# Kernel tuning notes

Measured on AMD Instinct MI355X. Metric: run time of the kernel, lower is better.

The kernel has to match this reference:

```python
import jax, jax.numpy as jnp
import numpy as np

N, E, DIN, DH, R = 50000, 1600000, 128, 128, 3


def setup_inputs() -> dict:
    key = jax.random.key(0)
    ks = jax.random.split(key, 32)
    inp = {}
    inp["x"] = jax.random.normal(ks[0], (N, DIN), jnp.float32)
    inp["h_prev"] = jax.random.normal(ks[1], (N, DH), jnp.float32)
    inp["edge_index"] = jax.random.randint(ks[2], (2, E), 0, N)
    inp["node_role"] = jax.random.randint(ks[3], (N,), 0, R)
    i = 4
    for name, din, has_b in (("xz", DIN, True), ("hz", DH, False), ("xr", DIN, True), ("hr", DH, False), ("xh", DIN, True), ("hh", DH, False)):
        inp[name + "_W"] = jax.random.normal(ks[i], (din, DH), jnp.float32) / np.float32(np.sqrt(din)); i += 1
        inp[name + "_Wg"] = jax.random.normal(ks[i], (R, DH), jnp.float32) * np.float32(0.1); i += 1
        inp[name + "_bg"] = jnp.zeros((R, DH), jnp.float32)
        inp[name + "_S"] = jax.random.normal(ks[i], (R, DH, DH), jnp.float32) / np.float32(np.sqrt(DH)); i += 1
        if has_b:
            inp[name + "_b"] = jnp.zeros((R, DH), jnp.float32)
    return inp


def _role_conv(x, W, Wg, bg, S, b, row, col, node_role):
    # x: [N, din] -> transformed features [N, DH]
    xt = x @ W
    r = node_role[row]                                  # role of source node per edge
    g = jax.nn.sigmoid(Wg[r] + bg[r])                   # [Etot, DH] role gate
    msg = xt[row] * g
    if b is not None:
        msg = msg + b[r]
    n = x.shape[0]
    summed = jax.ops.segment_sum(msg, col, num_segments=n)
    cnt = jax.ops.segment_sum(jnp.ones((row.shape[0],), xt.dtype), col, num_segments=n)
    aggr = summed / jnp.maximum(cnt, 1.0)[:, None]      # scatter_mean (self-loops ensure cnt>=1)
    # per-role self transform: out[i] = xt[i] @ S[role[i]] + aggr[i]
    out = aggr
    for nr in range(R):
        out = out + jnp.where((node_role == nr)[:, None], xt @ S[nr], jnp.float32(0.0))
    return jax.nn.relu(out)


def reference(x, edge_index, h_prev, node_role,
              xz_W, xz_Wg, xz_bg, xz_S, xz_b,
              hz_W, hz_Wg, hz_bg, hz_S,
              xr_W, xr_Wg, xr_bg, xr_S, xr_b,
              hr_W, hr_Wg, hr_bg, hr_S,
              xh_W, xh_Wg, xh_bg, xh_S, xh_b,
              hh_W, hh_Wg, hh_bg, hh_S):
    n = x.shape[0]
    loops = jnp.arange(n, dtype=edge_index.dtype)
    row = jnp.concatenate([edge_index[0], loops])       # add_self_loops appended at end
    col = jnp.concatenate([edge_index[1], loops])

    z = jax.nn.sigmoid(_role_conv(x, xz_W, xz_Wg, xz_bg, xz_S, xz_b, row, col, node_role)
                       + _role_conv(h_prev, hz_W, hz_Wg, hz_bg, hz_S, None, row, col, node_role))
    r = jax.nn.sigmoid(_role_conv(x, xr_W, xr_Wg, xr_bg, xr_S, xr_b, row, col, node_role)
                       + _role_conv(h_prev, hr_W, hr_Wg, hr_bg, hr_S, None, row, col, node_role))
    h_tilde = jnp.tanh(_role_conv(x, xh_W, xh_Wg, xh_bg, xh_S, xh_b, row, col, node_role)
                       + _role_conv(r * h_prev, hh_W, hh_Wg, hh_bg, hh_S, None, row, col, node_role))
    h_new = z * h_prev + (1.0 - z) * h_tilde
    return h_new
```

## Files before the change

### kernel.cpp

```cpp
#include <hip/hip_runtime.h>


typedef __bf16 bf16;
typedef __bf16 bf16x8 __attribute__((ext_vector_type(8)));
typedef float  f32x4  __attribute__((ext_vector_type(4)));
typedef float  f32x2  __attribute__((ext_vector_type(2)));
typedef unsigned char u8;

#define DH 128

__device__ __forceinline__ float sigmoidf_(float x) { return 1.0f / (1.0f + expf(-x)); }

__global__ __launch_bounds__(256) void hist_kernel(const int* __restrict__ ei, const int* __restrict__ role,
                                                   int* __restrict__ cnt3, int* __restrict__ rolecnt,
                                                   int E, int N)
{
  int i = blockIdx.x * 256 + threadIdx.x;
  int lane = threadIdx.x & 63;
  int r = (i < N) ? role[i] : -1;
  #pragma unroll
  for (int rr = 0; rr < 3; ++rr) {
    unsigned long long mask = __ballot(r == rr);
    if (lane == 0 && mask) atomicAdd(&rolecnt[rr], __popcll(mask));
  }
  if (i < E + N) {
    int src, dst;
    if (i < E) { src = ei[i]; dst = ei[E + i]; } else { src = i - E; dst = i - E; }
    int rs = (i < E) ? role[src] : r;
    if (i >= E) rs = role[i - E];
    atomicAdd(&cnt3[dst * 3 + rs], 1);
  }
}

__global__ __launch_bounds__(1024) void scan1_kernel(const int* __restrict__ cnt, int* __restrict__ off,
                                                     int* __restrict__ bsum, int n)
{
  __shared__ int wsum[16];
  int t = threadIdx.x, lane = t & 63, w = t >> 6;
  int idx = blockIdx.x * 1024 + t;
  int v = (idx < n) ? cnt[idx] : 0;
  int s = v;
  #pragma unroll
  for (int d = 1; d < 64; d <<= 1) { int u = __shfl_up(s, d); if (lane >= d) s += u; }
  if (lane == 63) wsum[w] = s;
  __syncthreads();
  if (w == 0 && lane < 16) {
    int ws = wsum[lane];
    #pragma unroll
    for (int d = 1; d < 16; d <<= 1) { int u = __shfl_up(ws, d); if (lane >= d) ws += u; }
    wsum[lane] = ws;
  }
  __syncthreads();
  int inc = ((w > 0) ? wsum[w - 1] : 0) + s;
  if (idx < n) off[idx + 1] = inc;
  if (t == 1023) bsum[blockIdx.x] = inc;
}

__global__ void scan2_kernel(int* __restrict__ bsum, int nb, const int* __restrict__ rolecnt,
                             int* __restrict__ rolefill, int* __restrict__ roleinfo)
{
  int lane = threadIdx.x;
  int carry = 0;
  for (int base = 0; base < nb; base += 64) {
    int v = (base + lane < nb) ? bsum[base + lane] : 0;
    int s = v;
    #pragma unroll
    for (int d = 1; d < 64; d <<= 1) { int u = __shfl_up(s, d); if (lane >= d) s += u; }
    if (base + lane < nb) bsum[base + lane] = carry + s - v;
    carry += __shfl(s, 63);
  }
  if (lane == 0) {
    int c0 = rolecnt[0], c1 = rolecnt[1], c2 = rolecnt[2];
    int s1 = (c0 + 255) & ~255;
    int s2 = s1 + ((c1 + 255) & ~255);
    int mp = s2 + ((c2 + 255) & ~255);
    rolefill[0] = 0; rolefill[1] = s1; rolefill[2] = s2;
    roleinfo[0] = s1; roleinfo[1] = s2;
    roleinfo[2] = c0;      roleinfo[3] = s1 - c0;
    roleinfo[4] = s1 + c1; roleinfo[5] = s2 - s1 - c1;
    roleinfo[6] = s2 + c2; roleinfo[7] = mp - s2 - c2;
  }
}

__global__ __launch_bounds__(1024) void scan3_kernel(int* __restrict__ off, int* __restrict__ fill,
                                                     const int* __restrict__ bsum, int n)
{
  int idx = blockIdx.x * 1024 + threadIdx.x;
  if (idx == 0) { off[0] = 0; fill[0] = 0; }
  if (idx < n) {
    int v = off[idx + 1] + bsum[blockIdx.x];
    off[idx + 1] = v;
    if (idx + 1 < n) fill[idx + 1] = v;
  }
}

__global__ void bucketinit_kernel(const int* __restrict__ off3, int* __restrict__ bucketfill,
                                  int NB, int W, int N)
{
  int b = blockIdx.x * 256 + threadIdx.x;
  if (b < NB) {
    int d = min(b * W, N);
    bucketfill[b] = off3[d * 3];
  }
}

__global__ __launch_bounds__(256) void partition_kernel(
    const int* __restrict__ ei, const int* __restrict__ spos,
    const int* __restrict__ roleinfo, int* __restrict__ bucketfill,
    int2* __restrict__ recs, int E, int N, int shiftB)
{
  __shared__ int lcnt[256], lbase[256];
  const int base = blockIdx.x * 4096;
  const int s1 = roleinfo[0], s2 = roleinfo[1];
  lcnt[threadIdx.x] = 0;
  __syncthreads();
  int myb[16], mybin[16], myt[16];
  #pragma unroll
  for (int k = 0; k < 16; ++k) {
    int i = base + k * 256 + threadIdx.x;
    myb[k] = -1;
    if (i < E + N) {
      int src, dst;
      if (i < E) { src = ei[i]; dst = ei[E + i]; } else { src = i - E; dst = i - E; }
      int t = spos[src];
      int r = (t >= s2) ? 2 : (t >= s1) ? 1 : 0;
      myb[k] = dst >> shiftB;
      mybin[k] = dst * 3 + r;
      myt[k] = t;
      atomicAdd(&lcnt[myb[k]], 1);
    }
  }
  __syncthreads();
  int c = lcnt[threadIdx.x];
  lbase[threadIdx.x] = (c > 0) ? atomicAdd(&bucketfill[threadIdx.x], c) : 0;
  __syncthreads();
  lcnt[threadIdx.x] = 0;
  __syncthreads();
  #pragma unroll
  for (int k = 0; k < 16; ++k) {
    if (myb[k] >= 0) {
      int slot = atomicAdd(&lcnt[myb[k]], 1);
      recs[lbase[myb[k]] + slot] = make_int2(mybin[k], myt[k]);
    }
  }
}

__global__ __launch_bounds__(1024) void binscatter_kernel(
    const int2* __restrict__ recs, const int* __restrict__ off3,
    int* __restrict__ fill3, int* __restrict__ ssrc, int W, int N)
{
  int b = blockIdx.x;
  int d0 = min(b * W, N), d1 = min((b + 1) * W, N);
  int s = off3[d0 * 3], e = off3[d1 * 3];
  for (int i = s + threadIdx.x; i < e; i += 1024) {
    int2 rec = recs[i];
    int pz = atomicAdd(&fill3[rec.x], 1);
    ssrc[pz] = rec.y;
  }
}

__global__ __launch_bounds__(256) void permscatter_kernel(const int* __restrict__ role, int* __restrict__ rolefill,
                                                          int* __restrict__ spos, int* __restrict__ sposinv, int N)
{
  int i = blockIdx.x * 256 + threadIdx.x;
  int lane = threadIdx.x & 63;
  int r = (i < N) ? role[i] : -1;
  #pragma unroll
  for (int rr = 0; rr < 3; ++rr) {
    unsigned long long mask = __ballot(r == rr);
    if (!mask) continue;
    int base = 0;
    if (lane == 0) base = atomicAdd(&rolefill[rr], __popcll(mask));
    base = __shfl(base, 0);
    if (r == rr) {
      int rank = (int)__popcll(mask & ((1ull << lane) - 1ull));
      int pos = base + rank;
      spos[i] = pos;
      sposinv[pos] = i;
    }
  }
}

__global__ __launch_bounds__(256) void zeropad_kernel(const int* __restrict__ roleinfo,
                                                      bf16* __restrict__ Ax, bf16* __restrict__ Ah)
{
  int id = blockIdx.x * 256 + threadIdx.x;
  int a = id / 49152, rem = id % 49152;
  int gp = rem / 16384, r2 = rem % 16384;
  int rr = r2 >> 6, c = r2 & 63;
  int gs = roleinfo[2 + gp * 2], gl = roleinfo[3 + gp * 2];
  if (rr < gl) {
    int row = gs + rr;
    size_t unit = (size_t)(row >> 4) * 1024 + c * 16 + (row & 15);
    bf16x8 z = {};
    ((bf16x8*)(a == 0 ? Ax : Ah))[unit] = z;
  }
}

__global__ __launch_bounds__(256) void prep_xh_kernel(const float* __restrict__ x, const float* __restrict__ h,
                                                      const int* __restrict__ spos, u8* __restrict__ xq8,
                                                      bf16* __restrict__ Ax, bf16* __restrict__ Ah, int N)
{
  int g = blockIdx.x * 256 + threadIdx.x;
  if (g >= N * 32) return;
  int n = g >> 5, j = g & 31;
  int t = spos[n];
  const float* src = (j < 16) ? (x + (size_t)n * 128 + (j << 3))
                              : (h + (size_t)n * 128 + ((j - 16) << 3));
  float4 v0 = ((const float4*)src)[0];
  float4 v1 = ((const float4*)src)[1];
  int lo = __builtin_amdgcn_cvt_pk_fp8_f32(v0.x, v0.y, 0, false);
  lo = __builtin_amdgcn_cvt_pk_fp8_f32(v0.z, v0.w, lo, true);
  int hi = __builtin_amdgcn_cvt_pk_fp8_f32(v1.x, v1.y, 0, false);
  hi = __builtin_amdgcn_cvt_pk_fp8_f32(v1.z, v1.w, hi, true);
  *(int2*)(xq8 + (size_t)t * 256 + j * 8) = make_int2(lo, hi);
  bf16x8 o;
  o[0] = (bf16)v0.x; o[1] = (bf16)v0.y; o[2] = (bf16)v0.z; o[3] = (bf16)v0.w;
  o[4] = (bf16)v1.x; o[5] = (bf16)v1.y; o[6] = (bf16)v1.z; o[7] = (bf16)v1.w;
  size_t unit = (size_t)(t >> 4) * 1024 + (48 + (j & 15)) * 16 + (t & 15);
  ((bf16x8*)(j < 16 ? Ax : Ah))[unit] = o;
}

struct PrepW { const float* W[6]; const float* Wg[6]; const float* bg[6]; };
__global__ __launch_bounds__(256) void prep_wf_kernel(PrepW pw, bf16* __restrict__ Wf)
{
  int idx = blockIdx.x * 256 + threadIdx.x;
  if (idx >= 294912) return;
  int cv = idx / 49152, pos = idx % 49152;
  int ks4q = pos >> 10;
  int col = (pos >> 3) & 127, j = pos & 7;
  int k = (ks4q >> 2) * 32 + (ks4q & 3) * 8 + j;
  int r = k >> 7, kk = k & 127;
  float g = sigmoidf_(pw.Wg[cv][r * 128 + col] + pw.bg[cv][r * 128 + col]);
  Wf[idx] = (bf16)(pw.W[cv][kk * 128 + col] * g);
}

struct PrepP { const float* W[6]; const float* S[6]; };
__global__ __launch_bounds__(128) void prep_pf_kernel(PrepP pp, bf16* __restrict__ Pf)
{
  int b = blockIdx.x;
  int cv = b / 384, rem = b % 384;
  int r = rem >> 7, kp = rem & 127;
  int col = threadIdx.x;
  const float* W = pp.W[cv] + (size_t)kp * 128;
  const float* S = pp.S[cv] + (size_t)r * 16384;
  float sum = 0.f;
  #pragma unroll 4
  for (int j2 = 0; j2 < 128; ++j2) sum += W[j2] * S[j2 * 128 + col];
  size_t o = (size_t)(cv * 3 + r) * 16384 + ((size_t)(kp >> 3) * 128 + col) * 8 + (kp & 7);
  Pf[o] = (bf16)sum;
}

#define ACCUM16(U, d) do { f32x2 f_;                                                   \
  f_ = __builtin_amdgcn_cvt_pk_f32_fp8((d).x, false); U[0]  += f_[0]; U[1]  += f_[1];  \
  f_ = __builtin_amdgcn_cvt_pk_f32_fp8((d).x, true);  U[2]  += f_[0]; U[3]  += f_[1];  \
  f_ = __builtin_amdgcn_cvt_pk_f32_fp8((d).y, false); U[4]  += f_[0]; U[5]  += f_[1];  \
  f_ = __builtin_amdgcn_cvt_pk_f32_fp8((d).y, true);  U[6]  += f_[0]; U[7]  += f_[1];  \
  f_ = __builtin_amdgcn_cvt_pk_f32_fp8((d).z, false); U[8]  += f_[0]; U[9]  += f_[1];  \
  f_ = __builtin_amdgcn_cvt_pk_f32_fp8((d).z, true);  U[10] += f_[0]; U[11] += f_[1];  \
  f_ = __builtin_amdgcn_cvt_pk_f32_fp8((d).w, false); U[12] += f_[0]; U[13] += f_[1];  \
  f_ = __builtin_amdgcn_cvt_pk_f32_fp8((d).w, true);  U[14] += f_[0]; U[15] += f_[1];  \
} while (0)

#define ACCSEL16(d, p) do {                      \
  if ((p) < o1)      { ACCUM16(u0, d); }         \
  else if ((p) < o2) { ACCUM16(u1, d); }         \
  else               { ACCUM16(u2, d); }         \
} while (0)

__global__ __launch_bounds__(512) void gather_xh_kernel(
    const u8* __restrict__ xq8, const int* __restrict__ off3, const int* __restrict__ ssrc,
    const int* __restrict__ sposinv, bf16* __restrict__ Ax, bf16* __restrict__ Ah,
    float4* __restrict__ cntf)
{
  __shared__ alignas(16) bf16 lds[8][768];
  int w = threadIdx.x >> 6, lane = threadIdx.x & 63;
  int t0 = blockIdx.x * 8;
  int t = t0 + w;
  int node = sposinv[t];
  int qt = lane >> 4, ql = lane & 15;

  if (node >= 0) {
    int o0 = __builtin_amdgcn_readfirstlane(off3[node * 3]);
    int o1 = __builtin_amdgcn_readfirstlane(off3[node * 3 + 1]);
    int o2 = __builtin_amdgcn_readfirstlane(off3[node * 3 + 2]);
    int o3 = __builtin_amdgcn_readfirstlane(off3[node * 3 + 3]);
    float inv = 1.0f / (float)(o3 - o0);
    const u8* base = xq8 + ql * 16;

    float u0[16], u1[16], u2[16];
    #pragma unroll
    for (int k = 0; k < 16; ++k) { u0[k] = 0.f; u1[k] = 0.f; u2[k] = 0.f; }

    const int e = o3, emax = o3 - 1;
    for (int i = o0; i < e; i += 16) {
      int p0 = i + qt, p1 = p0 + 4, p2 = p0 + 8, p3 = p0 + 12;
      int t0i = ssrc[min(p0, emax)];
      int t1i = ssrc[min(p1, emax)];
      int t2i = ssrc[min(p2, emax)];
      int t3i = ssrc[min(p3, emax)];
      int4 d0 = make_int4(0, 0, 0, 0), d1 = d0, d2 = d0, d3 = d0;
      if (p0 < e) d0 = *(const int4*)(base + (size_t)t0i * 256);
      if (p1 < e) d1 = *(const int4*)(base + (size_t)t1i * 256);
      if (p2 < e) d2 = *(const int4*)(base + (size_t)t2i * 256);
      if (p3 < e) d3 = *(const int4*)(base + (size_t)t3i * 256);
      ACCSEL16(d0, p0);
      ACCSEL16(d1, p1);
      ACCSEL16(d2, p2);
      ACCSEL16(d3, p3);
    }

    #pragma unroll
    for (int k = 0; k < 16; ++k) {
      u0[k] += __shfl_xor(u0[k], 16); u0[k] += __shfl_xor(u0[k], 32);
      u1[k] += __shfl_xor(u1[k], 16); u1[k] += __shfl_xor(u1[k], 32);
      u2[k] += __shfl_xor(u2[k], 16); u2[k] += __shfl_xor(u2[k], 32);
    }
    if (qt == 0) {
      bf16x8 p0v, p1v;
      int sb0 = (ql < 8) ? (ql * 16) : (384 + (ql - 8) * 16);
      #pragma unroll
      for (int k = 0; k < 8; ++k) { p0v[k] = (bf16)(u0[k] * inv); p1v[k] = (bf16)(u0[8 + k] * inv); }
      *(bf16x8*)&lds[w][sb0] = p0v;
      *(bf16x8*)&lds[w][sb0 + 8] = p1v;
      #pragma unroll
      for (int k = 0; k < 8; ++k) { p0v[k] = (bf16)(u1[k] * inv); p1v[k] = (bf16)(u1[8 + k] * inv); }
      *(bf16x8*)&lds[w][sb0 + 128] = p0v;
      *(bf16x8*)&lds[w][sb0 + 136] = p1v;
      #pragma unroll
      for (int k = 0; k < 8; ++k) { p0v[k] = (bf16)(u2[k] * inv); p1v[k] = (bf16)(u2[8 + k] * inv); }
      *(bf16x8*)&lds[w][sb0 + 256] = p0v;
      *(bf16x8*)&lds[w][sb0 + 264] = p1v;
    }
    if (lane == 0)
      cntf[t] = make_float4((o1 - o0) * inv, (o2 - o1) * inv, (o3 - o2) * inv, (float)(o3 - o0));
  } else {
    if (lane < 48) {
      bf16x8 z = {};
      *(bf16x8*)&lds[w][lane * 16] = z;
      *(bf16x8*)&lds[w][lane * 16 + 8] = z;
    }
    if (lane == 0) cntf[t] = make_float4(0.f, 0.f, 0.f, 0.f);
  }

  __syncthreads();

  int tid = threadIdx.x;
  if (tid < 384) {
    int lc = tid >> 3, row = tid & 7;
    size_t unit = (size_t)(t0 >> 4) * 1024 + lc * 16 + (t0 & 15) + row;
    __builtin_nontemporal_store(*(const bf16x8*)&lds[row][lc * 8], (bf16x8*)Ax + unit);
    __builtin_nontemporal_store(*(const bf16x8*)&lds[row][384 + lc * 8], (bf16x8*)Ah + unit);
  }
}

#define ACCUM8(U, d) do { f32x2 f_;                                                  \
  f_ = __builtin_amdgcn_cvt_pk_f32_fp8((d).x, false); U[0] += f_[0]; U[1] += f_[1];  \
  f_ = __builtin_amdgcn_cvt_pk_f32_fp8((d).x, true);  U[2] += f_[0]; U[3] += f_[1];  \
  f_ = __builtin_amdgcn_cvt_pk_f32_fp8((d).y, false); U[4] += f_[0]; U[5] += f_[1];  \
  f_ = __builtin_amdgcn_cvt_pk_f32_fp8((d).y, true);  U[6] += f_[0]; U[7] += f_[1];  \
} while (0)

#define ACCSEL8(d, p) do {                      \
  if ((p) < o1)      { ACCUM8(v0, d); }         \
  else if ((p) < o2) { ACCUM8(v1, d); }         \
  else               { ACCUM8(v2, d); }         \
} while (0)

__global__ __launch_bounds__(512) void gather_q_kernel(
    const u8* __restrict__ q8, const int* __restrict__ off3, const int* __restrict__ ssrc,
    const int* __restrict__ sposinv, bf16* __restrict__ Aq)
{
  __shared__ alignas(16) bf16 lds[8][384];
  int w = threadIdx.x >> 6, lane = threadIdx.x & 63;
  int t0 = blockIdx.x * 8;
  int t = t0 + w;
  int node = sposinv[t];
  int qt = lane >> 4, ql = lane & 15;

  if (node >= 0) {
    int o0 = __builtin_amdgcn_readfirstlane(off3[node * 3]);
    int o1 = __builtin_amdgcn_readfirstlane(off3[node * 3 + 1]);
    int o2 = __builtin_amdgcn_readfirstlane(off3[node * 3 + 2]);
    int o3 = __builtin_amdgcn_readfirstlane(off3[node * 3 + 3]);
    float inv = 1.0f / (float)(o3 - o0);
    const u8* base = q8 + ql * 8;

    float v0[8], v1[8], v2[8];
    #pragma unroll
    for (int k = 0; k < 8; ++k) { v0[k] = 0.f; v1[k] = 0.f; v2[k] = 0.f; }

    const int e = o3, emax = o3 - 1;
    for (int i = o0; i < e; i += 16) {
      int p0 = i + qt, p1 = p0 + 4, p2 = p0 + 8, p3 = p0 + 12;
      int t0i = ssrc[min(p0, emax)];
      int t1i = ssrc[min(p1, emax)];
      int t2i = ssrc[min(p2, emax)];
      int t3i = ssrc[min(p3, emax)];
      int2 d0 = make_int2(0, 0), d1 = d0, d2 = d0, d3 = d0;
      if (p0 < e) d0 = *(const int2*)(base + (size_t)t0i * 128);
      if (p1 < e) d1 = *(const int2*)(base + (size_t)t1i * 128);
      if (p2 < e) d2 = *(const int2*)(base + (size_t)t2i * 128);
      if (p3 < e) d3 = *(const int2*)(base + (size_t)t3i * 128);
      ACCSEL8(d0, p0);
      ACCSEL8(d1, p1);
      ACCSEL8(d2, p2);
      ACCSEL8(d3, p3);
    }

    #pragma unroll
    for (int k = 0; k < 8; ++k) {
      v0[k] += __shfl_xor(v0[k], 16); v0[k] += __shfl_xor(v0[k], 32);
      v1[k] += __shfl_xor(v1[k], 16); v1[k] += __shfl_xor(v1[k], 32);
      v2[k] += __shfl_xor(v2[k], 16); v2[k] += __shfl_xor(v2[k], 32);
    }
    if (qt == 0) {
      bf16x8 pk;
      #pragma unroll
      for (int k = 0; k < 8; ++k) pk[k] = (bf16)(v0[k] * inv);
      *(bf16x8*)&lds[w][ql * 8] = pk;
      #pragma unroll
      for (int k = 0; k < 8; ++k) pk[k] = (bf16)(v1[k] * inv);
      *(bf16x8*)&lds[w][128 + ql * 8] = pk;
      #pragma unroll
      for (int k = 0; k < 8; ++k) pk[k] = (bf16)(v2[k] * inv);
      *(bf16x8*)&lds[w][256 + ql * 8] = pk;
    }
  } else {
    if (lane < 48) {
      bf16x8 z = {};
      *(bf16x8*)&lds[w][lane * 8] = z;
    }
  }

  __syncthreads();

  int tid = threadIdx.x;
  if (tid < 384) {
    int lc = tid >> 3, row = tid & 7;
    size_t unit = (size_t)(t0 >> 4) * 1024 + lc * 16 + (t0 & 15) + row;
    __builtin_nontemporal_store(*(const bf16x8*)&lds[row][lc * 8], (bf16x8*)Aq + unit);
  }
}

struct GArgs {
  const bf16* Ap[5];
  const bf16* wf[5];
  const bf16* pf[5];
  bf16* out[5];
  const float* bias[5];
};

__global__ __launch_bounds__(256, 3) void gemm_kernel(GArgs ga, const float4* __restrict__ cntf,
                                                      const int* __restrict__ roleinfo)
{
  const int cv = blockIdx.y;
  const bf16* __restrict__ Ap = ga.Ap[cv];
  const bf16* __restrict__ wf = ga.wf[cv];
  const bf16* __restrict__ pf = ga.pf[cv];
  bf16* __restrict__ out = ga.out[cv];
  const float* __restrict__ bias = ga.bias[cv];

  const int w = threadIdx.x >> 6, lane = threadIdx.x & 63;
  const int q = lane >> 4, l = lane & 15;
  const int rb0 = blockIdx.x * 8 + w * 2;
  const int row0 = blockIdx.x * 128;
  const int s1 = roleinfo[0], s2 = roleinfo[1];
  const int role = (row0 >= s2) ? 2 : (row0 >= s1) ? 1 : 0;
  const int laneoff = q * 128 + l;

  f32x4 acc[2][8];
  #pragma unroll
  for (int j = 0; j < 2; ++j)
    #pragma unroll
    for (int ct = 0; ct < 8; ++ct)
      #pragma unroll
      for (int k = 0; k < 4; ++k) acc[j][ct][k] = 0.f;

  const bf16x8* A0 = (const bf16x8*)Ap + (size_t)rb0 * 1024 + lane;
  const bf16x8* WF = (const bf16x8*)wf + laneoff;
  const bf16x8* PF = (const bf16x8*)pf + role * 2048 + laneoff;

  #pragma unroll 2
  for (int ks = 0; ks < 16; ++ks) {
    const bf16x8* bp = (ks < 12) ? (WF + ks * 512) : (PF + (ks - 12) * 512);
    bf16x8 a0 = A0[ks * 64];
    bf16x8 a1 = A0[1024 + ks * 64];
    #pragma unroll
    for (int ct = 0; ct < 8; ++ct) {
      bf16x8 b = bp[ct * 16];
      acc[0][ct] = __builtin_amdgcn_mfma_f32_16x16x32_bf16(a0, b, acc[0][ct], 0, 0, 0);
      acc[1][ct] = __builtin_amdgcn_mfma_f32_16x16x32_bf16(a1, b, acc[1][ct], 0, 0, 0);
    }
  }

  const bool hb = (bias != nullptr);
  #pragma unroll
  for (int j = 0; j < 2; ++j) {
    int rb = rb0 + j;
    float4 cfs[4];
    if (hb) {
      #pragma unroll
      for (int reg = 0; reg < 4; ++reg) cfs[reg] = cntf[rb * 16 + q * 4 + reg];
    }
    #pragma unroll
    for (int ct = 0; ct < 8; ++ct) {
      int col = ct * 16 + l;
      float b0 = 0, b1 = 0, b2 = 0;
      if (hb) { b0 = bias[col]; b1 = bias[128 + col]; b2 = bias[256 + col]; }
      #pragma unroll
      for (int reg = 0; reg < 4; ++reg) {
        int t = rb * 16 + q * 4 + reg;
        float v = acc[j][ct][reg];
        if (hb) v += cfs[reg].x * b0 + cfs[reg].y * b1 + cfs[reg].z * b2;
        out[(size_t)t * 128 + col] = (bf16)fmaxf(v, 0.f);
      }
    }
  }
}

__global__ __launch_bounds__(256) void combine1_kernel(
    const bf16* __restrict__ o0, const bf16* __restrict__ o1,
    const bf16* __restrict__ o2, const bf16* __restrict__ o3,
    const float* __restrict__ h, const int* __restrict__ spos,
    float* __restrict__ zbuf, u8* __restrict__ q8, bf16* __restrict__ Aq, int N)
{
  int g = blockIdx.x * 256 + threadIdx.x;
  if (g >= N * 16) return;
  int n = g >> 4, o = g & 15;
  int t = spos[n];
  size_t tb = (size_t)t * 16 + o;
  bf16x8 a0 = ((const bf16x8*)o0)[tb];
  bf16x8 a1 = ((const bf16x8*)o1)[tb];
  bf16x8 a2 = ((const bf16x8*)o2)[tb];
  bf16x8 a3 = ((const bf16x8*)o3)[tb];
  size_t nb = (size_t)n * 16 + o;
  float4 h0 = ((const float4*)h)[nb * 2];
  float4 h1 = ((const float4*)h)[nb * 2 + 1];
  float hv[8] = {h0.x, h0.y, h0.z, h0.w, h1.x, h1.y, h1.z, h1.w};
  float zv[8], qv[8];
  bf16x8 qb;
  #pragma unroll
  for (int j = 0; j < 8; ++j) {
    zv[j] = sigmoidf_((float)a0[j] + (float)a1[j]);
    qv[j] = sigmoidf_((float)a2[j] + (float)a3[j]) * hv[j];
    qb[j] = (bf16)qv[j];
  }
  ((float4*)zbuf)[nb * 2]     = make_float4(zv[0], zv[1], zv[2], zv[3]);
  ((float4*)zbuf)[nb * 2 + 1] = make_float4(zv[4], zv[5], zv[6], zv[7]);
  int lo = __builtin_amdgcn_cvt_pk_fp8_f32(qv[0], qv[1], 0, false);
  lo = __builtin_amdgcn_cvt_pk_fp8_f32(qv[2], qv[3], lo, true);
  int hi = __builtin_amdgcn_cvt_pk_fp8_f32(qv[4], qv[5], 0, false);
  hi = __builtin_amdgcn_cvt_pk_fp8_f32(qv[6], qv[7], hi, true);
  *(int2*)(q8 + (size_t)t * 128 + o * 8) = make_int2(lo, hi);
  size_t unit = (size_t)(t >> 4) * 1024 + (48 + o) * 16 + (t & 15);
  ((bf16x8*)Aq)[unit] = qb;
}

__global__ __launch_bounds__(256) void combine2_kernel(
    const float* __restrict__ zbuf, const bf16* __restrict__ o4, const bf16* __restrict__ o5,
    const float* __restrict__ h, const int* __restrict__ spos, float* __restrict__ out, int N)
{
  int g = blockIdx.x * 256 + threadIdx.x;
  if (g >= N * 16) return;
  int n = g >> 4, o = g & 15;
  int t = spos[n];
  size_t tb = (size_t)t * 16 + o;
  bf16x8 a = ((const bf16x8*)o4)[tb];
  bf16x8 b = ((const bf16x8*)o5)[tb];
  size_t nb = (size_t)n * 16 + o;
  float4 z0 = ((const float4*)zbuf)[nb * 2];
  float4 z1 = ((const float4*)zbuf)[nb * 2 + 1];
  float4 h0 = ((const float4*)h)[nb * 2];
  float4 h1 = ((const float4*)h)[nb * 2 + 1];
  float zv[8] = {z0.x, z0.y, z0.z, z0.w, z1.x, z1.y, z1.z, z1.w};
  float hv[8] = {h0.x, h0.y, h0.z, h0.w, h1.x, h1.y, h1.z, h1.w};
  float ov[8];
  #pragma unroll
  for (int j = 0; j < 8; ++j)
    ov[j] = zv[j] * hv[j] + (1.f - zv[j]) * tanhf((float)a[j] + (float)b[j]);
  ((float4*)out)[nb * 2]     = make_float4(ov[0], ov[1], ov[2], ov[3]);
  ((float4*)out)[nb * 2 + 1] = make_float4(ov[4], ov[5], ov[6], ov[7]);
}

extern "C" void kernel_launch(void* const* d_in, const int* in_sizes, int n_in,
                              void* d_out, int out_size, void* d_ws, size_t ws_size,
                              hipStream_t stream)
{
  (void)n_in; (void)out_size; (void)ws_size;
  const float* x    = (const float*)d_in[0];
  const float* h    = (const float*)d_in[1];
  const int*   ei   = (const int*)d_in[2];
  const int*   role = (const int*)d_in[3];
  const int N = in_sizes[0] / DH;
  const int E = in_sizes[2] / 2;
  const int Etot = E + N;
  const int rows_pad = ((N + 765) + 255) & ~255;
  const int gx = rows_pad / 128;
  const int n3 = N * 3;
  const int nb3 = (n3 + 1023) / 1024;

  int shiftB = 8;
  while (((N - 1) >> shiftB) >= 256) ++shiftB;
  const int W = 1 << shiftB;
  const int NB = (N + W - 1) >> shiftB;

  static const int Wi[6]  = {4, 9, 13, 18, 22, 27};
  static const int Wgi[6] = {5, 10, 14, 19, 23, 28};
  static const int bgi[6] = {6, 11, 15, 20, 24, 29};
  static const int Si[6]  = {7, 12, 16, 21, 25, 30};

  char* p = (char*)d_ws;
  auto alloc = [&](size_t bytes) -> char* {
    char* r = p;
    p += (bytes + 255) & ~(size_t)255;
    return r;
  };

  bf16* Ax = (bf16*)alloc((size_t)rows_pad * 512 * 2);
  bf16* Ah = (bf16*)alloc((size_t)rows_pad * 512 * 2);
  bf16* Aq = Ax;
  u8* xq8  = (u8*)alloc((size_t)rows_pad * 256);
  u8* q8   = (u8*)alloc((size_t)rows_pad * 128);
  bf16* outs[6];
  for (int c = 0; c < 5; ++c) outs[c] = (bf16*)alloc((size_t)rows_pad * 128 * 2);
  outs[5] = outs[0];
  float* zbuf = (float*)alloc((size_t)N * 128 * 4);
  float4* cntf = (float4*)alloc((size_t)rows_pad * 16);
  bf16* Wf = (bf16*)alloc((size_t)6 * 49152 * 2);
  bf16* Pf = (bf16*)alloc((size_t)18 * 16384 * 2);
  int* cnt3  = (int*)alloc((size_t)n3 * 4);
  int* off3  = (int*)alloc((size_t)(n3 + 1) * 4);
  int* fill3 = (int*)alloc((size_t)n3 * 4);
  int* bsum  = (int*)alloc((size_t)(nb3 + 1) * 4);
  int* ssrc  = (int*)alloc((size_t)Etot * 4);
  int2* recs = (int2*)alloc((size_t)Etot * 8);
  int* spos  = (int*)alloc((size_t)N * 4);
  int* sposinv = (int*)alloc((size_t)rows_pad * 4);
  int* rolecnt  = (int*)alloc(64);
  int* rolefill = (int*)alloc(64);
  int* roleinfo = (int*)alloc(64);
  int* bucketfill = (int*)alloc((size_t)(NB + 1) * 4);

  hipMemsetAsync(cnt3, 0, (size_t)n3 * 4, stream);
  hipMemsetAsync(rolecnt, 0, 16, stream);
  hipMemsetAsync(sposinv, 0xFF, (size_t)rows_pad * 4, stream);

  int egrid = (Etot + 255) / 256;
  int ngrid = (N + 255) / 256;
  hist_kernel<<<egrid, 256, 0, stream>>>(ei, role, cnt3, rolecnt, E, N);
  scan1_kernel<<<nb3, 1024, 0, stream>>>(cnt3, off3, bsum, n3);
  scan2_kernel<<<1, 64, 0, stream>>>(bsum, nb3, rolecnt, rolefill, roleinfo);
  scan3_kernel<<<nb3, 1024, 0, stream>>>(off3, fill3, bsum, n3);
  permscatter_kernel<<<ngrid, 256, 0, stream>>>(role, rolefill, spos, sposinv, N);
  bucketinit_kernel<<<1, 256, 0, stream>>>(off3, bucketfill, NB, W, N);
  partition_kernel<<<(Etot + 4095) / 4096, 256, 0, stream>>>(ei, spos, roleinfo, bucketfill,
                                                             recs, E, N, shiftB);
  binscatter_kernel<<<NB, 1024, 0, stream>>>(recs, off3, fill3, ssrc, W, N);
  zeropad_kernel<<<384, 256, 0, stream>>>(roleinfo, Ax, Ah);

  prep_xh_kernel<<<(N * 32 + 255) / 256, 256, 0, stream>>>(x, h, spos, xq8, Ax, Ah, N);

  PrepW pw;
  for (int c = 0; c < 6; ++c) {
    pw.W[c] = (const float*)d_in[Wi[c]];
    pw.Wg[c] = (const float*)d_in[Wgi[c]];
    pw.bg[c] = (const float*)d_in[bgi[c]];
  }
  prep_wf_kernel<<<1152, 256, 0, stream>>>(pw, Wf);
  PrepP pp;
  for (int c = 0; c < 6; ++c) { pp.W[c] = (const float*)d_in[Wi[c]]; pp.S[c] = (const float*)d_in[Si[c]]; }
  prep_pf_kernel<<<2304, 128, 0, stream>>>(pp, Pf);

  gather_xh_kernel<<<rows_pad / 8, 512, 0, stream>>>(xq8, off3, ssrc, sposinv, Ax, Ah, cntf);

  GArgs g0;
  { int cvs[5] = {0, 2, 4, 1, 3};
    static const int bi2[5] = {8, 17, 26, -1, -1};
    const bf16* Apts[5] = {Ax, Ax, Ax, Ah, Ah};
    for (int k = 0; k < 5; ++k) {
      int c = cvs[k];
      g0.Ap[k] = Apts[k];
      g0.wf[k] = Wf + (size_t)c * 49152;
      g0.pf[k] = Pf + (size_t)c * 3 * 16384;
      g0.out[k] = outs[c];
      g0.bias[k] = (bi2[k] >= 0) ? (const float*)d_in[bi2[k]] : nullptr;
    } }
  gemm_kernel<<<dim3(gx, 5), 256, 0, stream>>>(g0, cntf, roleinfo);

  combine1_kernel<<<(N * 16 + 255) / 256, 256, 0, stream>>>(outs[0], outs[1], outs[2], outs[3],
                                                            h, spos, zbuf, q8, Aq, N);

  gather_q_kernel<<<rows_pad / 8, 512, 0, stream>>>(q8, off3, ssrc, sposinv, Aq);

  GArgs g2 = {};
  g2.Ap[0] = Aq;
  g2.wf[0] = Wf + (size_t)5 * 49152;
  g2.pf[0] = Pf + (size_t)5 * 3 * 16384;
  g2.out[0] = outs[5];
  g2.bias[0] = nullptr;
  gemm_kernel<<<dim3(gx, 1), 256, 0, stream>>>(g2, cntf, roleinfo);

  combine2_kernel<<<(N * 16 + 255) / 256, 256, 0, stream>>>(zbuf, outs[4], outs[5], h, spos,
                                                            (float*)d_out, N);
}
```

Before: 682.3 us.

## Split fp8 gather features into 64-byte column chunks across grid y

The fp8 copies of x/h and q are rearranged into column-chunked planes of 64 bytes per row. The gather kernels are launched with a second grid dimension (4 chunks for xh, 2 for q), so each block gathers only one chunk and each lane loads 4 bytes instead of 16 or 8. The aim is better L2 locality, since each gathered plane is smaller, plus lower register use and more blocks for parallelism. In exchange, the edge-index reads and segment offset reads are repeated once per chunk.

```diff
diff --git a/kernel.cpp b/kernel.cpp
--- a/kernel.cpp
+++ b/kernel.cpp
@@ -3,6 +3,7 @@
 
 typedef __bf16 bf16;
 typedef __bf16 bf16x8 __attribute__((ext_vector_type(8)));
+typedef __bf16 bf16x4 __attribute__((ext_vector_type(4)));
 typedef float  f32x4  __attribute__((ext_vector_type(4)));
 typedef float  f32x2  __attribute__((ext_vector_type(2)));
 typedef unsigned char u8;
@@ -198,8 +199,9 @@
 }
 
 __global__ __launch_bounds__(256) void prep_xh_kernel(const float* __restrict__ x, const float* __restrict__ h,
-                                                      const int* __restrict__ spos, u8* __restrict__ xq8,
-                                                      bf16* __restrict__ Ax, bf16* __restrict__ Ah, int N)
+                                                      const int* __restrict__ spos, u8* __restrict__ xq8c,
+                                                      bf16* __restrict__ Ax, bf16* __restrict__ Ah,
+                                                      int N, int rows_pad)
 {
   int g = blockIdx.x * 256 + threadIdx.x;
   if (g >= N * 32) return;
@@ -213,7 +215,7 @@
   lo = __builtin_amdgcn_cvt_pk_fp8_f32(v0.z, v0.w, lo, true);
   int hi = __builtin_amdgcn_cvt_pk_fp8_f32(v1.x, v1.y, 0, false);
   hi = __builtin_amdgcn_cvt_pk_fp8_f32(v1.z, v1.w, hi, true);
-  *(int2*)(xq8 + (size_t)t * 256 + j * 8) = make_int2(lo, hi);
+  *(int2*)(xq8c + ((size_t)(j >> 3) * rows_pad + t) * 64 + (j & 7) * 8) = make_int2(lo, hi);
   bf16x8 o;
   o[0] = (bf16)v0.x; o[1] = (bf16)v0.y; o[2] = (bf16)v0.z; o[3] = (bf16)v0.w;
   o[4] = (bf16)v1.x; o[5] = (bf16)v1.y; o[6] = (bf16)v1.z; o[7] = (bf16)v1.w;
@@ -251,30 +253,25 @@
   Pf[o] = (bf16)sum;
 }
 
-#define ACCUM16(U, d) do { f32x2 f_;                                                   \
-  f_ = __builtin_amdgcn_cvt_pk_f32_fp8((d).x, false); U[0]  += f_[0]; U[1]  += f_[1];  \
-  f_ = __builtin_amdgcn_cvt_pk_f32_fp8((d).x, true);  U[2]  += f_[0]; U[3]  += f_[1];  \
-  f_ = __builtin_amdgcn_cvt_pk_f32_fp8((d).y, false); U[4]  += f_[0]; U[5]  += f_[1];  \
-  f_ = __builtin_amdgcn_cvt_pk_f32_fp8((d).y, true);  U[6]  += f_[0]; U[7]  += f_[1];  \
-  f_ = __builtin_amdgcn_cvt_pk_f32_fp8((d).z, false); U[8]  += f_[0]; U[9]  += f_[1];  \
-  f_ = __builtin_amdgcn_cvt_pk_f32_fp8((d).z, true);  U[10] += f_[0]; U[11] += f_[1];  \
-  f_ = __builtin_amdgcn_cvt_pk_f32_fp8((d).w, false); U[12] += f_[0]; U[13] += f_[1];  \
-  f_ = __builtin_amdgcn_cvt_pk_f32_fp8((d).w, true);  U[14] += f_[0]; U[15] += f_[1];  \
+#define ACCUM4(U, d) do { f32x2 f_;                                                \
+  f_ = __builtin_amdgcn_cvt_pk_f32_fp8((d), false); U[0] += f_[0]; U[1] += f_[1];  \
+  f_ = __builtin_amdgcn_cvt_pk_f32_fp8((d), true);  U[2] += f_[0]; U[3] += f_[1];  \
 } while (0)
 
-#define ACCSEL16(d, p) do {                      \
-  if ((p) < o1)      { ACCUM16(u0, d); }         \
-  else if ((p) < o2) { ACCUM16(u1, d); }         \
-  else               { ACCUM16(u2, d); }         \
+#define ACCSEL4(d, p) do {                      \
+  if ((p) < o1)      { ACCUM4(u0, d); }         \
+  else if ((p) < o2) { ACCUM4(u1, d); }         \
+  else               { ACCUM4(u2, d); }         \
 } while (0)
 
 __global__ __launch_bounds__(512) void gather_xh_kernel(
-    const u8* __restrict__ xq8, const int* __restrict__ off3, const int* __restrict__ ssrc,
+    const u8* __restrict__ xq8c, const int* __restrict__ off3, const int* __restrict__ ssrc,
     const int* __restrict__ sposinv, bf16* __restrict__ Ax, bf16* __restrict__ Ah,
-    float4* __restrict__ cntf)
-{
-  __shared__ alignas(16) bf16 lds[8][768];
+    float4* __restrict__ cntf, int rows_pad)
+{
+  __shared__ alignas(16) bf16 lds[8][192];
   int w = threadIdx.x >> 6, lane = threadIdx.x & 63;
+  int c = blockIdx.y;
   int t0 = blockIdx.x * 8;
   int t = t0 + w;
   int node = sposinv[t];
@@ -286,11 +283,11 @@
     int o2 = __builtin_amdgcn_readfirstlane(off3[node * 3 + 2]);
     int o3 = __builtin_amdgcn_readfirstlane(off3[node * 3 + 3]);
     float inv = 1.0f / (float)(o3 - o0);
-    const u8* base = xq8 + ql * 16;
-
-    float u0[16], u1[16], u2[16];
-    #pragma unroll
-    for (int k = 0; k < 16; ++k) { u0[k] = 0.f; u1[k] = 0.f; u2[k] = 0.f; }
+    const u8* base = xq8c + (size_t)c * rows_pad * 64 + ql * 4;
+
+    float u0[4], u1[4], u2[4];
+    #pragma unroll
+    for (int k = 0; k < 4; ++k) { u0[k] = 0.f; u1[k] = 0.f; u2[k] = 0.f; }
 
     const int e = o3, emax = o3 - 1;
     for (int i = o0; i < e; i += 16) {
@@ -299,80 +296,65 @@
       int t1i = ssrc[min(p1, emax)];
       int t2i = ssrc[min(p2, emax)];
       int t3i = ssrc[min(p3, emax)];
-      int4 d0 = make_int4(0, 0, 0, 0), d1 = d0, d2 = d0, d3 = d0;
-      if (p0 < e) d0 = *(const int4*)(base + (size_t)t0i * 256);
-      if (p1 < e) d1 = *(const int4*)(base + (size_t)t1i * 256);
-      if (p2 < e) d2 = *(const int4*)(base + (size_t)t2i * 256);
-      if (p3 < e) d3 = *(const int4*)(base + (size_t)t3i * 256);
-      ACCSEL16(d0, p0);
-      ACCSEL16(d1, p1);
-      ACCSEL16(d2, p2);
-      ACCSEL16(d3, p3);
-    }
-
-    #pragma unroll
-    for (int k = 0; k < 16; ++k) {
+      int d0 = 0, d1 = 0, d2 = 0, d3 = 0;
+      if (p0 < e) d0 = *(const int*)(base + (size_t)t0i * 64);
+      if (p1 < e) d1 = *(const int*)(base + (size_t)t1i * 64);
+      if (p2 < e) d2 = *(const int*)(base + (size_t)t2i * 64);
+      if (p3 < e) d3 = *(const int*)(base + (size_t)t3i * 64);
+      ACCSEL4(d0, p0);
+      ACCSEL4(d1, p1);
+      ACCSEL4(d2, p2);
+      ACCSEL4(d3, p3);
+    }
+
+    #pragma unroll
+    for (int k = 0; k < 4; ++k) {
       u0[k] += __shfl_xor(u0[k], 16); u0[k] += __shfl_xor(u0[k], 32);
       u1[k] += __shfl_xor(u1[k], 16); u1[k] += __shfl_xor(u1[k], 32);
       u2[k] += __shfl_xor(u2[k], 16); u2[k] += __shfl_xor(u2[k], 32);
     }
     if (qt == 0) {
-      bf16x8 p0v, p1v;
-      int sb0 = (ql < 8) ? (ql * 16) : (384 + (ql - 8) * 16);
-      #pragma unroll
-      for (int k = 0; k < 8; ++k) { p0v[k] = (bf16)(u0[k] * inv); p1v[k] = (bf16)(u0[8 + k] * inv); }
-      *(bf16x8*)&lds[w][sb0] = p0v;
-      *(bf16x8*)&lds[w][sb0 + 8] = p1v;
-      #pragma unroll
-      for (int k = 0; k < 8; ++k) { p0v[k] = (bf16)(u1[k] * inv); p1v[k] = (bf16)(u1[8 + k] * inv); }
-      *(bf16x8*)&lds[w][sb0 + 128] = p0v;
-      *(bf16x8*)&lds[w][sb0 + 136] = p1v;
-      #pragma unroll
-      for (int k = 0; k < 8; ++k) { p0v[k] = (bf16)(u2[k] * inv); p1v[k] = (bf16)(u2[8 + k] * inv); }
-      *(bf16x8*)&lds[w][sb0 + 256] = p0v;
-      *(bf16x8*)&lds[w][sb0 + 264] = p1v;
-    }
-    if (lane == 0)
+      bf16x4 pk;
+      #pragma unroll
+      for (int k = 0; k < 4; ++k) pk[k] = (bf16)(u0[k] * inv);
+      *(bf16x4*)&lds[w][ql * 4] = pk;
+      #pragma unroll
+      for (int k = 0; k < 4; ++k) pk[k] = (bf16)(u1[k] * inv);
+      *(bf16x4*)&lds[w][64 + ql * 4] = pk;
+      #pragma unroll
+      for (int k = 0; k < 4; ++k) pk[k] = (bf16)(u2[k] * inv);
+      *(bf16x4*)&lds[w][128 + ql * 4] = pk;
+    }
+    if (lane == 0 && c == 0)
       cntf[t] = make_float4((o1 - o0) * inv, (o2 - o1) * inv, (o3 - o2) * inv, (float)(o3 - o0));
   } else {
-    if (lane < 48) {
+    if (lane < 24) {
       bf16x8 z = {};
-      *(bf16x8*)&lds[w][lane * 16] = z;
-      *(bf16x8*)&lds[w][lane * 16 + 8] = z;
-    }
-    if (lane == 0) cntf[t] = make_float4(0.f, 0.f, 0.f, 0.f);
+      *(bf16x8*)&lds[w][lane * 8] = z;
+    }
+    if (lane == 0 && c == 0) cntf[t] = make_float4(0.f, 0.f, 0.f, 0.f);
   }
 
   __syncthreads();
 
   int tid = threadIdx.x;
-  if (tid < 384) {
-    int lc = tid >> 3, row = tid & 7;
-    size_t unit = (size_t)(t0 >> 4) * 1024 + lc * 16 + (t0 & 15) + row;
-    __builtin_nontemporal_store(*(const bf16x8*)&lds[row][lc * 8], (bf16x8*)Ax + unit);
-    __builtin_nontemporal_store(*(const bf16x8*)&lds[row][384 + lc * 8], (bf16x8*)Ah + unit);
-  }
-}
-
-#define ACCUM8(U, d) do { f32x2 f_;                                                  \
-  f_ = __builtin_amdgcn_cvt_pk_f32_fp8((d).x, false); U[0] += f_[0]; U[1] += f_[1];  \
-  f_ = __builtin_amdgcn_cvt_pk_f32_fp8((d).x, true);  U[2] += f_[0]; U[3] += f_[1];  \
-  f_ = __builtin_amdgcn_cvt_pk_f32_fp8((d).y, false); U[4] += f_[0]; U[5] += f_[1];  \
-  f_ = __builtin_amdgcn_cvt_pk_f32_fp8((d).y, true);  U[6] += f_[0]; U[7] += f_[1];  \
-} while (0)
-
-#define ACCSEL8(d, p) do {                      \
-  if ((p) < o1)      { ACCUM8(v0, d); }         \
-  else if ((p) < o2) { ACCUM8(v1, d); }         \
-  else               { ACCUM8(v2, d); }         \
-} while (0)
+  if (tid < 192) {
+    int lc2 = tid >> 3, row = tid & 7;
+    int rr = lc2 >> 3, j = lc2 & 7;
+    int col = rr * 16 + (c & 1) * 8 + j;
+    size_t unit = (size_t)(t0 >> 4) * 1024 + col * 16 + (t0 & 15) + row;
+    bf16* dst = (c < 2) ? Ax : Ah;
+    __builtin_nontemporal_store(*(const bf16x8*)&lds[row][lc2 * 8], (bf16x8*)dst + unit);
+  }
+}
 
 __global__ __launch_bounds__(512) void gather_q_kernel(
-    const u8* __restrict__ q8, const int* __restrict__ off3, const int* __restrict__ ssrc,
-    const int* __restrict__ sposinv, bf16* __restrict__ Aq)
-{
-  __shared__ alignas(16) bf16 lds[8][384];
+    const u8* __restrict__ q8c, const int* __restrict__ off3, const int* __restrict__ ssrc,
+    const int* __restrict__ sposinv, bf16* __restrict__ Aq, int rows_pad)
+{
+  __shared__ alignas(16) bf16 lds[8][192];
   int w = threadIdx.x >> 6, lane = threadIdx.x & 63;
+  int c = blockIdx.y;
   int t0 = blockIdx.x * 8;
   int t = t0 + w;
   int node = sposinv[t];
@@ -384,11 +366,11 @@
     int o2 = __builtin_amdgcn_readfirstlane(off3[node * 3 + 2]);
     int o3 = __builtin_amdgcn_readfirstlane(off3[node * 3 + 3]);
     float inv = 1.0f / (float)(o3 - o0);
-    const u8* base = q8 + ql * 8;
-
-    float v0[8], v1[8], v2[8];
-    #pragma unroll
-    for (int k = 0; k < 8; ++k) { v0[k] = 0.f; v1[k] = 0.f; v2[k] = 0.f; }
+    const u8* base = q8c + (size_t)c * rows_pad * 64 + ql * 4;
+
+    float u0[4], u1[4], u2[4];
+    #pragma unroll
+    for (int k = 0; k < 4; ++k) { u0[k] = 0.f; u1[k] = 0.f; u2[k] = 0.f; }
 
     const int e = o3, emax = o3 - 1;
     for (int i = o0; i < e; i += 16) {
@@ -397,37 +379,37 @@
       int t1i = ssrc[min(p1, emax)];
       int t2i = ssrc[min(p2, emax)];
       int t3i = ssrc[min(p3, emax)];
-      int2 d0 = make_int2(0, 0), d1 = d0, d2 = d0, d3 = d0;
-      if (p0 < e) d0 = *(const int2*)(base + (size_t)t0i * 128);
-      if (p1 < e) d1 = *(const int2*)(base + (size_t)t1i * 128);
-      if (p2 < e) d2 = *(const int2*)(base + (size_t)t2i * 128);
-      if (p3 < e) d3 = *(const int2*)(base + (size_t)t3i * 128);
-      ACCSEL8(d0, p0);
-      ACCSEL8(d1, p1);
-      ACCSEL8(d2, p2);
-      ACCSEL8(d3, p3);
-    }
-
-    #pragma unroll
-    for (int k = 0; k < 8; ++k) {
-      v0[k] += __shfl_xor(v0[k], 16); v0[k] += __shfl_xor(v0[k], 32);
-      v1[k] += __shfl_xor(v1[k], 16); v1[k] += __shfl_xor(v1[k], 32);
-      v2[k] += __shfl_xor(v2[k], 16); v2[k] += __shfl_xor(v2[k], 32);
+      int d0 = 0, d1 = 0, d2 = 0, d3 = 0;
+      if (p0 < e) d0 = *(const int*)(base + (size_t)t0i * 64);
+      if (p1 < e) d1 = *(const int*)(base + (size_t)t1i * 64);
+      if (p2 < e) d2 = *(const int*)(base + (size_t)t2i * 64);
+      if (p3 < e) d3 = *(const int*)(base + (size_t)t3i * 64);
+      ACCSEL4(d0, p0);
+      ACCSEL4(d1, p1);
+      ACCSEL4(d2, p2);
+      ACCSEL4(d3, p3);
+    }
+
+    #pragma unroll
+    for (int k = 0; k < 4; ++k) {
+      u0[k] += __shfl_xor(u0[k], 16); u0[k] += __shfl_xor(u0[k], 32);
+      u1[k] += __shfl_xor(u1[k], 16); u1[k] += __shfl_xor(u1[k], 32);
+      u2[k] += __shfl_xor(u2[k], 16); u2[k] += __shfl_xor(u2[k], 32);
     }
     if (qt == 0) {
-      bf16x8 pk;
-      #pragma unroll
-      for (int k = 0; k < 8; ++k) pk[k] = (bf16)(v0[k] * inv);
-      *(bf16x8*)&lds[w][ql * 8] = pk;
-      #pragma unroll
-      for (int k = 0; k < 8; ++k) pk[k] = (bf16)(v1[k] * inv);
-      *(bf16x8*)&lds[w][128 + ql * 8] = pk;
-      #pragma unroll
-      for (int k = 0; k < 8; ++k) pk[k] = (bf16)(v2[k] * inv);
-      *(bf16x8*)&lds[w][256 + ql * 8] = pk;
+      bf16x4 pk;
+      #pragma unroll
+      for (int k = 0; k < 4; ++k) pk[k] = (bf16)(u0[k] * inv);
+      *(bf16x4*)&lds[w][ql * 4] = pk;
+      #pragma unroll
+      for (int k = 0; k < 4; ++k) pk[k] = (bf16)(u1[k] * inv);
+      *(bf16x4*)&lds[w][64 + ql * 4] = pk;
+      #pragma unroll
+      for (int k = 0; k < 4; ++k) pk[k] = (bf16)(u2[k] * inv);
+      *(bf16x4*)&lds[w][128 + ql * 4] = pk;
     }
   } else {
-    if (lane < 48) {
+    if (lane < 24) {
       bf16x8 z = {};
       *(bf16x8*)&lds[w][lane * 8] = z;
     }
@@ -436,10 +418,12 @@
   __syncthreads();
 
   int tid = threadIdx.x;
-  if (tid < 384) {
-    int lc = tid >> 3, row = tid & 7;
-    size_t unit = (size_t)(t0 >> 4) * 1024 + lc * 16 + (t0 & 15) + row;
-    __builtin_nontemporal_store(*(const bf16x8*)&lds[row][lc * 8], (bf16x8*)Aq + unit);
+  if (tid < 192) {
+    int lc2 = tid >> 3, row = tid & 7;
+    int rr = lc2 >> 3, j = lc2 & 7;
+    int col = rr * 16 + c * 8 + j;
+    size_t unit = (size_t)(t0 >> 4) * 1024 + col * 16 + (t0 & 15) + row;
+    __builtin_nontemporal_store(*(const bf16x8*)&lds[row][lc2 * 8], (bf16x8*)Aq + unit);
   }
 }
 
@@ -523,7 +507,7 @@
     const bf16* __restrict__ o0, const bf16* __restrict__ o1,
     const bf16* __restrict__ o2, const bf16* __restrict__ o3,
     const float* __restrict__ h, const int* __restrict__ spos,
-    float* __restrict__ zbuf, u8* __restrict__ q8, bf16* __restrict__ Aq, int N)
+    float* __restrict__ zbuf, u8* __restrict__ q8c, bf16* __restrict__ Aq, int N, int rows_pad)
 {
   int g = blockIdx.x * 256 + threadIdx.x;
   if (g >= N * 16) return;
@@ -552,7 +536,7 @@
   lo = __builtin_amdgcn_cvt_pk_fp8_f32(qv[2], qv[3], lo, true);
   int hi = __builtin_amdgcn_cvt_pk_fp8_f32(qv[4], qv[5], 0, false);
   hi = __builtin_amdgcn_cvt_pk_fp8_f32(qv[6], qv[7], hi, true);
-  *(int2*)(q8 + (size_t)t * 128 + o * 8) = make_int2(lo, hi);
+  *(int2*)(q8c + ((size_t)(o >> 3) * rows_pad + t) * 64 + (o & 7) * 8) = make_int2(lo, hi);
   size_t unit = (size_t)(t >> 4) * 1024 + (48 + o) * 16 + (t & 15);
   ((bf16x8*)Aq)[unit] = qb;
 }
@@ -659,7 +643,7 @@
   binscatter_kernel<<<NB, 1024, 0, stream>>>(recs, off3, fill3, ssrc, W, N);
   zeropad_kernel<<<384, 256, 0, stream>>>(roleinfo, Ax, Ah);
 
-  prep_xh_kernel<<<(N * 32 + 255) / 256, 256, 0, stream>>>(x, h, spos, xq8, Ax, Ah, N);
+  prep_xh_kernel<<<(N * 32 + 255) / 256, 256, 0, stream>>>(x, h, spos, xq8, Ax, Ah, N, rows_pad);
 
   PrepW pw;
   for (int c = 0; c < 6; ++c) {
@@ -672,7 +656,8 @@
   for (int c = 0; c < 6; ++c) { pp.W[c] = (const float*)d_in[Wi[c]]; pp.S[c] = (const float*)d_in[Si[c]]; }
   prep_pf_kernel<<<2304, 128, 0, stream>>>(pp, Pf);
 
-  gather_xh_kernel<<<rows_pad / 8, 512, 0, stream>>>(xq8, off3, ssrc, sposinv, Ax, Ah, cntf);
+  gather_xh_kernel<<<dim3(rows_pad / 8, 4), 512, 0, stream>>>(xq8, off3, ssrc, sposinv,
+                                                              Ax, Ah, cntf, rows_pad);
 
   GArgs g0;
   { int cvs[5] = {0, 2, 4, 1, 3};
@@ -689,9 +674,9 @@
   gemm_kernel<<<dim3(gx, 5), 256, 0, stream>>>(g0, cntf, roleinfo);
 
   combine1_kernel<<<(N * 16 + 255) / 256, 256, 0, stream>>>(outs[0], outs[1], outs[2], outs[3],
-                                                            h, spos, zbuf, q8, Aq, N);
-
-  gather_q_kernel<<<rows_pad / 8, 512, 0, stream>>>(q8, off3, ssrc, sposinv, Aq);
+                                                            h, spos, zbuf, q8, Aq, N, rows_pad);
+
+  gather_q_kernel<<<dim3(rows_pad / 8, 2), 512, 0, stream>>>(q8, off3, ssrc, sposinv, Aq, rows_pad);
 
   GArgs g2 = {};
   g2.Ap[0] = Aq;
```

Result: slower. 736.4 us (+7.9%).
